# Optimization experiments

Hardware: AMD Instinct MI355X
Metric: run time of the kernel (lower is better)

## Reference

```python
import jax, jax.numpy as jnp
import numpy as np

KERNEL_SIZE = 3
FILTERS = 512


def setup_inputs() -> dict:
    key = jax.random.key(0)
    k1, k2 = jax.random.split(key)
    B, T, D, K, F = 8, 2048, 512, KERNEL_SIZE, FILTERS
    x = jax.random.normal(k1, (B, T, D), dtype=jnp.float32)
    kernels = jax.random.normal(k2, (B, T, K, F), dtype=jnp.float32)
    return {"x": x, "kernels": kernels}


def reference(x, kernels):
    # x: [B, T, D], kernels: [B, T, K, F] -> out: [B, T, F]
    B, T, D = x.shape
    K = kernels.shape[2]
    pad = K // 2
    xp = jnp.pad(x, ((0, 0), (pad, pad), (0, 0)))  # [B, T+2*pad, D]
    # Sliding windows along T: patches[b, t, k, d] = xp[b, t + k, d]
    patches = jnp.stack([xp[:, k:k + T, :] for k in range(K)], axis=2)  # [B, T, K, D]
    # Faithful to tf.einsum('btkd,btkf->btf'): sums over BOTH k and d.
    out = jnp.einsum('btkd,btkf->btf', patches, kernels)
    return out
```

## Files before the change

kernel.cpp:

```cpp
#include <hip/hip_runtime.h>
#include <hip/hip_bf16.h>


#define B_ 8
#define T_ 2048
#define D_ 512
#define F_ 512

__global__ __launch_bounds__(256) void rowsum_kernel(
    const float* __restrict__ x, float* __restrict__ S) {
    const int row  = blockIdx.x * 4 + (threadIdx.x >> 6);
    const int lane = threadIdx.x & 63;
    const float4* xr = (const float4*)(x + (size_t)row * D_);
    float4 a = xr[lane];
    float4 b = xr[lane + 64];
    float s = (a.x + a.y) + (a.z + a.w) + (b.x + b.y) + (b.z + b.w);
    #pragma unroll
    for (int off = 32; off > 0; off >>= 1)
        s += __shfl_down(s, off, 64);
    if (lane == 0) S[row] = s;
}

__global__ __launch_bounds__(128) void conv_kernel(
    const float* __restrict__ kern, const float* __restrict__ S,
    float* __restrict__ out) {
    const int bt = blockIdx.x;
    const int t  = bt & (T_ - 1);

    const float s0 = (t > 0)      ? S[bt - 1] : 0.0f;
    const float s1 = S[bt];
    const float s2 = (t < T_ - 1) ? S[bt + 1] : 0.0f;

    const float4* kr = (const float4*)(kern + (size_t)bt * 3 * F_);
    const int i = threadIdx.x;
    float4 k0 = kr[i];
    float4 k1 = kr[i + F_ / 4];
    float4 k2 = kr[i + 2 * (F_ / 4)];

    float4 o;
    o.x = s0 * k0.x + s1 * k1.x + s2 * k2.x;
    o.y = s0 * k0.y + s1 * k1.y + s2 * k2.y;
    o.z = s0 * k0.z + s1 * k1.z + s2 * k2.z;
    o.w = s0 * k0.w + s1 * k1.w + s2 * k2.w;

    ((float4*)(out + (size_t)bt * F_))[i] = o;
}

extern "C" void kernel_launch(void* const* d_in, const int* in_sizes, int n_in,
                              void* d_out, int out_size, void* d_ws, size_t ws_size,
                              hipStream_t stream) {
    const float* x    = (const float*)d_in[0];
    const float* kern = (const float*)d_in[1];
    float* out = (float*)d_out;
    float* S   = (float*)d_ws;

    const int rows = B_ * T_;
    rowsum_kernel<<<rows / 4, 256, 0, stream>>>(x, S);
    conv_kernel<<<rows, 128, 0, stream>>>(kern, S, out);
}
```

Before: 178.3 us.

## Fuse row-sum and conv into one kernel with 8-timestep tiles

Replaces the two-kernel pipeline (row sums to workspace, then per-timestep conv) with a single kernel. Each block computes the row sums for 8 timesteps plus halo rows into shared memory and applies them to the kernel weights. This removes a launch and the global round trip of the sums, and gives each thread more independent loads in flight. In exchange it re-reads halo rows of x and adds a block barrier.

```diff
diff --git a/kernel.cpp b/kernel.cpp
--- a/kernel.cpp
+++ b/kernel.cpp
@@ -6,44 +6,73 @@
 #define T_ 2048
 #define D_ 512
 #define F_ 512
+#define TT 8
+#define NROWS (TT + 2)
 
-__global__ __launch_bounds__(256) void rowsum_kernel(
-    const float* __restrict__ x, float* __restrict__ S) {
-    const int row  = blockIdx.x * 4 + (threadIdx.x >> 6);
-    const int lane = threadIdx.x & 63;
-    const float4* xr = (const float4*)(x + (size_t)row * D_);
-    float4 a = xr[lane];
-    float4 b = xr[lane + 64];
-    float s = (a.x + a.y) + (a.z + a.w) + (b.x + b.y) + (b.z + b.w);
+__global__ __launch_bounds__(256) void fused_conv_kernel(
+    const float* __restrict__ x, const float* __restrict__ kern,
+    float* __restrict__ out) {
+    __shared__ float Ss[NROWS];
+
+    const int tid  = threadIdx.x;
+    const int wave = tid >> 6;
+    const int lane = tid & 63;
+    const int bt0  = blockIdx.x * TT;
+    const int t0   = bt0 & (T_ - 1);
+
+    float4 va[3], vb[3];
     #pragma unroll
-    for (int off = 32; off > 0; off >>= 1)
-        s += __shfl_down(s, off, 64);
-    if (lane == 0) S[row] = s;
-}
+    for (int i = 0; i < 3; ++i) {
+        const int r  = wave + i * 4;
+        const int gt = t0 + r - 1;
+        va[i] = make_float4(0.f, 0.f, 0.f, 0.f);
+        vb[i] = make_float4(0.f, 0.f, 0.f, 0.f);
+        if (r < NROWS && gt >= 0 && gt < T_) {
+            const float4* xr = (const float4*)(x + (size_t)(bt0 + r - 1) * D_);
+            va[i] = xr[lane];
+            vb[i] = xr[lane + 64];
+        }
+    }
 
-__global__ __launch_bounds__(128) void conv_kernel(
-    const float* __restrict__ kern, const float* __restrict__ S,
-    float* __restrict__ out) {
-    const int bt = blockIdx.x;
-    const int t  = bt & (T_ - 1);
+    const int f4  = tid & 127;
+    const int tl0 = tid >> 7;
+    float4 kk[4][3];
+    #pragma unroll
+    for (int it = 0; it < 4; ++it) {
+        const int tl = it * 2 + tl0;
+        const float4* kr = (const float4*)(kern + (size_t)(bt0 + tl) * (3 * F_));
+        kk[it][0] = kr[f4];
+        kk[it][1] = kr[f4 + 128];
+        kk[it][2] = kr[f4 + 256];
+    }
 
-    const float s0 = (t > 0)      ? S[bt - 1] : 0.0f;
-    const float s1 = S[bt];
-    const float s2 = (t < T_ - 1) ? S[bt + 1] : 0.0f;
+    #pragma unroll
+    for (int i = 0; i < 3; ++i) {
+        const int r = wave + i * 4;
+        if (r < NROWS) {
+            float s = (va[i].x + va[i].y) + (va[i].z + va[i].w)
+                    + (vb[i].x + vb[i].y) + (vb[i].z + vb[i].w);
+            #pragma unroll
+            for (int off = 32; off > 0; off >>= 1)
+                s += __shfl_down(s, off, 64);
+            if (lane == 0) Ss[r] = s;
+        }
+    }
+    __syncthreads();
 
-    const float4* kr = (const float4*)(kern + (size_t)bt * 3 * F_);
-    const int i = threadIdx.x;
-    float4 k0 = kr[i];
-    float4 k1 = kr[i + F_ / 4];
-    float4 k2 = kr[i + 2 * (F_ / 4)];
-
-    float4 o;
-    o.x = s0 * k0.x + s1 * k1.x + s2 * k2.x;
-    o.y = s0 * k0.y + s1 * k1.y + s2 * k2.y;
-    o.z = s0 * k0.z + s1 * k1.z + s2 * k2.z;
-    o.w = s0 * k0.w + s1 * k1.w + s2 * k2.w;
-
-    ((float4*)(out + (size_t)bt * F_))[i] = o;
+    #pragma unroll
+    for (int it = 0; it < 4; ++it) {
+        const int tl = it * 2 + tl0;
+        const float s0 = Ss[tl];
+        const float s1 = Ss[tl + 1];
+        const float s2 = Ss[tl + 2];
+        float4 o;
+        o.x = s0 * kk[it][0].x + s1 * kk[it][1].x + s2 * kk[it][2].x;
+        o.y = s0 * kk[it][0].y + s1 * kk[it][1].y + s2 * kk[it][2].y;
+        o.z = s0 * kk[it][0].z + s1 * kk[it][1].z + s2 * kk[it][2].z;
+        o.w = s0 * kk[it][0].w + s1 * kk[it][1].w + s2 * kk[it][2].w;
+        ((float4*)(out + (size_t)(bt0 + tl) * F_))[f4] = o;
+    }
 }
 
 extern "C" void kernel_launch(void* const* d_in, const int* in_sizes, int n_in,
@@ -52,9 +81,7 @@
     const float* x    = (const float*)d_in[0];
     const float* kern = (const float*)d_in[1];
     float* out = (float*)d_out;
-    float* S   = (float*)d_ws;
 
-    const int rows = B_ * T_;
-    rowsum_kernel<<<rows / 4, 256, 0, stream>>>(x, S);
-    conv_kernel<<<rows, 128, 0, stream>>>(kern, S, out);
+    const int blocks = (B_ * T_) / TT;
+    fused_conv_kernel<<<blocks, 256, 0, stream>>>(x, kern, out);
 }
```

Result: no change. 180.2 us (+1.1%).
